# Performance work log

Measured on AMD Instinct MI355X. Metric: run time of the kernel, lower is better.

## Reference

```python
import jax, jax.numpy as jnp
import numpy as np

ESP = 1e-10  # matches SRKNN.ESP
K = 16       # top-k neighbors


def _logmap(x):
    # sign-preserving log map (repo helper not shown; eps matches SRKNN.ESP)
    return jnp.sign(x) * jnp.log(jnp.abs(x) + ESP)


def setup_inputs() -> dict:
    key = jax.random.key(0)
    k1, k2, k3, k4 = jax.random.split(key, 4)
    B, C, H, W = 2, 128, 32, 32
    C2 = C // 2
    X = jax.random.normal(k1, (B, C, H, W), jnp.float32)
    # nn.Linear(C, C//2, bias=False) weights, torch layout [out, in]
    W_min = jax.random.normal(k2, (C2, C), jnp.float32) * 0.08
    W_sub = jax.random.normal(k3, (C2, C), jnp.float32) * 0.08
    M = jax.random.normal(k4, (C2, C2), jnp.float32)
    return {"X": X, "W_min": W_min, "W_sub": W_sub, "M": M}


def reference(X, W_min, W_sub, M):
    B, C, H, W = X.shape
    XV = jnp.transpose(X, (0, 2, 3, 1)).reshape(B, -1, C)  # [B, N, C]
    N = XV.shape[1]
    # project then log-map; pairwise (i=minuend, j=subtrahend) without repeat
    pm = _logmap(XV @ W_min.T)  # [B, N, C2]
    ps = _logmap(XV @ W_sub.T)  # [B, N, C2]
    subR = jax.nn.sigmoid(pm[:, :, None, :] - ps[:, None, :, :])  # [B, N, N, C2]
    A = M.T @ M  # [C2, C2] learned Mahalanobis metric
    dis = jnp.sqrt(jnp.sum(jnp.einsum('bijc,cd->bijd', subR, A) * subR, axis=-1))  # [B,N,N]
    diff = jax.nn.sigmoid(-dis)
    value, index = jax.lax.top_k(diff, K)  # [B, N, K]
    value = -value.reshape(B, -1, 1)       # [B, N*K, 1]
    index = index.reshape(B, -1)           # [B, N*K]
    return index, value
```

## Files before the change

kernel.cpp:

```cpp
#include <hip/hip_runtime.h>
#include <hip/hip_bf16.h>
#include <hip/hip_fp16.h>
#include <math.h>

#define NN 1024
#define CC 128
#define C2 64
#define KK 16
#define NCAND 24

#if __has_builtin(__builtin_amdgcn_exp2f)
#define EXP2F(x) __builtin_amdgcn_exp2f(x)
#else
#define EXP2F(x) exp2f(x)
#endif
#define LOG2E 1.4426950408889634f

typedef __fp16  hf2   __attribute__((ext_vector_type(2)));
typedef _Float16 half8 __attribute__((ext_vector_type(8)));
typedef float f32x4    __attribute__((ext_vector_type(4)));
typedef int   int4v    __attribute__((ext_vector_type(4)));
typedef unsigned int uint;

__device__ __forceinline__ float fast_rcp(float x) {
    return __builtin_amdgcn_rcpf(x);
}

#define LDS_FENCE() do { \
    asm volatile("s_waitcnt lgkmcnt(0)" ::: "memory"); \
    __builtin_amdgcn_sched_barrier(0); } while (0)

__global__ __launch_bounds__(128) void proj_buildA(
        const float* __restrict__ X,
        const float* __restrict__ Wm,
        const float* __restrict__ Ws,
        const float* __restrict__ M,
        float* __restrict__ pm,
        float* __restrict__ ps,
        float* __restrict__ psE,
        float* __restrict__ A) {
    if (blockIdx.x >= 2 * NN) {
        const int e = (blockIdx.x - 2 * NN) * 128 + threadIdx.x;
        const int c = e >> 6, d = e & 63;
        float acc = 0.f;
        #pragma unroll 8
        for (int r = 0; r < C2; ++r)
            acc = fmaf(M[r * C2 + c], M[r * C2 + d], acc);
        A[e] = acc;
        return;
    }

    const int bn = blockIdx.x;
    const int b  = bn >> 10;
    const int n  = bn & (NN - 1);
    const int t  = threadIdx.x;

    __shared__ float xv[CC];
    xv[t] = X[b * CC * NN + t * NN + n];
    __syncthreads();

    const int d = t & (C2 - 1);
    const float* wr = ((t < C2) ? Wm : Ws) + d * CC;
    float acc = 0.f;
    #pragma unroll
    for (int c = 0; c < CC; ++c)
        acc = fmaf(wr[c], xv[c], acc);

    float a = __fadd_rn(fabsf(acc), 1e-10f);
    float l = logf(a);
    float r = (acc > 0.f) ? l : ((acc < 0.f) ? -l : 0.f);
    if (t < C2) {
        pm[bn * C2 + d] = r;
    } else {
        ps[bn * C2 + d] = r;
        psE[bn * C2 + d] = EXP2F(r * LOG2E);
    }
}

#define SIGF16(PMEF, Y0, Y1, BF) do {                                         \
    float s0 = PMEF[0] * fast_rcp(PMEF[0] + (Y0).x);                          \
    float s1 = PMEF[1] * fast_rcp(PMEF[1] + (Y0).y);                          \
    float s2 = PMEF[2] * fast_rcp(PMEF[2] + (Y0).z);                          \
    float s3 = PMEF[3] * fast_rcp(PMEF[3] + (Y0).w);                          \
    float s4 = PMEF[4] * fast_rcp(PMEF[4] + (Y1).x);                          \
    float s5 = PMEF[5] * fast_rcp(PMEF[5] + (Y1).y);                          \
    float s6 = PMEF[6] * fast_rcp(PMEF[6] + (Y1).z);                          \
    float s7 = PMEF[7] * fast_rcp(PMEF[7] + (Y1).w);                          \
    hf2 p0 = __builtin_amdgcn_cvt_pkrtz(s0, s1);                              \
    hf2 p1 = __builtin_amdgcn_cvt_pkrtz(s2, s3);                              \
    hf2 p2 = __builtin_amdgcn_cvt_pkrtz(s4, s5);                              \
    hf2 p3 = __builtin_amdgcn_cvt_pkrtz(s6, s7);                              \
    int4v iv = { __builtin_bit_cast(int, p0), __builtin_bit_cast(int, p1),    \
                 __builtin_bit_cast(int, p2), __builtin_bit_cast(int, p3) };  \
    BF = __builtin_bit_cast(half8, iv);                                       \
} while (0)

#define MFMA4(AC, KT, B)                                                              \
    AC[0] = __builtin_amdgcn_mfma_f32_16x16x32_f16(af[0][KT], B, AC[0], 0, 0, 0);     \
    AC[1] = __builtin_amdgcn_mfma_f32_16x16x32_f16(af[1][KT], B, AC[1], 0, 0, 0);     \
    AC[2] = __builtin_amdgcn_mfma_f32_16x16x32_f16(af[2][KT], B, AC[2], 0, 0, 0);     \
    AC[3] = __builtin_amdgcn_mfma_f32_16x16x32_f16(af[3][KT], B, AC[3], 0, 0, 0);

#define STREAM(PMEF, T0, T1, T2, T3, AC) do {                                 \
    half8 b0, b1;                                                             \
    SIGF16(PMEF[0], T0, T1, b0);                                              \
    SIGF16(PMEF[1], T2, T3, b1);                                              \
    MFMA4(AC, 0, b0)                                                          \
    MFMA4(AC, 1, b1)                                                          \
} while (0)

#define SQUARE16(AC, S) do {                                                  \
    _Pragma("unroll")                                                         \
    for (int e = 0; e < 4; ++e) {                                             \
        S = fmaf(AC[0][e], AC[0][e], S);                                      \
        S = fmaf(AC[1][e], AC[1][e], S);                                      \
        S = fmaf(AC[2][e], AC[2][e], S);                                      \
        S = fmaf(AC[3][e], AC[3][e], S);                                      \
    }                                                                         \
} while (0)

__global__ __launch_bounds__(256, 2) void pair_topk(
        const float* __restrict__ pm,
        const float* __restrict__ ps,
        const float* __restrict__ psE,
        const float* __restrict__ Mf,
        const float* __restrict__ A,
        float* __restrict__ out) {
    const int tid  = threadIdx.x;
    const int wv   = tid >> 6;
    const int lane = tid & 63;
    const int g    = lane >> 4;
    const int lj   = lane & 15;

    const int rbase = blockIdx.x * 4;
    const int b     = rbase >> 10;

    __shared__ uint  d2u[4][NN];
    __shared__ float sC[4][2][C2];
    __shared__ float cdiffL[4][NCAND];

    const float* psb  = ps  + b * NN * C2;
    const float* psEb = psE + b * NN * C2;

    {
        float pmEf[4][2][8];
        #pragma unroll
        for (int r = 0; r < 4; ++r) {
            #pragma unroll
            for (int kt = 0; kt < 2; ++kt) {
                const float4 a0 = *(const float4*)(pm + (rbase + r) * C2 + kt * 32 + g * 8);
                const float4 a1 = *(const float4*)(pm + (rbase + r) * C2 + kt * 32 + g * 8 + 4);
                pmEf[r][kt][0] = EXP2F(a0.x * LOG2E); pmEf[r][kt][1] = EXP2F(a0.y * LOG2E);
                pmEf[r][kt][2] = EXP2F(a0.z * LOG2E); pmEf[r][kt][3] = EXP2F(a0.w * LOG2E);
                pmEf[r][kt][4] = EXP2F(a1.x * LOG2E); pmEf[r][kt][5] = EXP2F(a1.y * LOG2E);
                pmEf[r][kt][6] = EXP2F(a1.z * LOG2E); pmEf[r][kt][7] = EXP2F(a1.w * LOG2E);
            }
        }

        half8 af[4][2];
        #pragma unroll
        for (int rt = 0; rt < 4; ++rt) {
            #pragma unroll
            for (int kt = 0; kt < 2; ++kt) {
                const float* mrow = Mf + (rt * 16 + lj) * C2 + kt * 32 + g * 8;
                const float4 m0 = *(const float4*)mrow;
                const float4 m1 = *(const float4*)(mrow + 4);
                float mv[8] = {m0.x, m0.y, m0.z, m0.w, m1.x, m1.y, m1.z, m1.w};
                #pragma unroll
                for (int e = 0; e < 8; ++e)
                    af[rt][kt][e] = (_Float16)mv[e];
            }
        }

        const int tbase = wv * 16;
        const float* p0 = psEb + (long)((tbase + 0) * 16 + lj) * C2 + g * 8;
        float4 c0 = *(const float4*)(p0);      float4 c1 = *(const float4*)(p0 + 4);
        float4 c2 = *(const float4*)(p0 + 32); float4 c3 = *(const float4*)(p0 + 36);

        #pragma unroll 1
        for (int it = 0; it < 16; ++it) {
            float4 n0, n1, n2, n3;
            if (it < 15) {
                const float* q0 = psEb + (long)((tbase + it + 1) * 16 + lj) * C2 + g * 8;
                n0 = *(const float4*)(q0);      n1 = *(const float4*)(q0 + 4);
                n2 = *(const float4*)(q0 + 32); n3 = *(const float4*)(q0 + 36);
            }

            f32x4 ac0[4] = {{0,0,0,0},{0,0,0,0},{0,0,0,0},{0,0,0,0}};
            f32x4 ac1[4] = {{0,0,0,0},{0,0,0,0},{0,0,0,0},{0,0,0,0}};
            f32x4 ac2[4] = {{0,0,0,0},{0,0,0,0},{0,0,0,0},{0,0,0,0}};
            f32x4 ac3[4] = {{0,0,0,0},{0,0,0,0},{0,0,0,0},{0,0,0,0}};

            __builtin_amdgcn_s_setprio(1);
            STREAM(pmEf[0], c0, c1, c2, c3, ac0);
            STREAM(pmEf[1], c0, c1, c2, c3, ac1);
            STREAM(pmEf[2], c0, c1, c2, c3, ac2);
            STREAM(pmEf[3], c0, c1, c2, c3, ac3);
            __builtin_amdgcn_s_setprio(0);

            float s0 = 0.f, s1 = 0.f, s2 = 0.f, s3 = 0.f;
            SQUARE16(ac0, s0);
            SQUARE16(ac1, s1);
            SQUARE16(ac2, s2);
            SQUARE16(ac3, s3);
            s0 += __shfl_xor(s0, 16, 64); s0 += __shfl_xor(s0, 32, 64);
            s1 += __shfl_xor(s1, 16, 64); s1 += __shfl_xor(s1, 32, 64);
            s2 += __shfl_xor(s2, 16, 64); s2 += __shfl_xor(s2, 32, 64);
            s3 += __shfl_xor(s3, 16, 64); s3 += __shfl_xor(s3, 32, 64);
            if (lane < 16) {
                const int jj = (tbase + it) * 16 + lane;
                d2u[0][jj] = (__float_as_uint(s0) & 0xFFFFFC00u) | (uint)jj;
                d2u[1][jj] = (__float_as_uint(s1) & 0xFFFFFC00u) | (uint)jj;
                d2u[2][jj] = (__float_as_uint(s2) & 0xFFFFFC00u) | (uint)jj;
                d2u[3][jj] = (__float_as_uint(s3) & 0xFFFFFC00u) | (uint)jj;
            }

            c0 = n0; c1 = n1; c2 = n2; c3 = n3;
        }
    }
    __syncthreads();

    const int bi = rbase + wv;
    const int i  = bi & (NN - 1);
    const float pm_own = pm[bi * C2 + lane];

    uint v[16];
    #pragma unroll
    for (int q = 0; q < 16; ++q) v[q] = d2u[wv][q * 64 + lane];

    int myCand = 0;
    #pragma unroll 1
    for (int k = 0; k < NCAND; ++k) {
        uint bv = v[0];
        #pragma unroll
        for (int q = 1; q < 16; ++q) bv = min(bv, v[q]);
        #pragma unroll
        for (int st = 0; st < 6; ++st)
            bv = min(bv, (uint)__shfl_xor((int)bv, 1 << st, 64));
        #pragma unroll
        for (int q = 0; q < 16; ++q)
            if (v[q] == bv) v[q] = 0xFFFFFFFFu;
        if (lane == k) myCand = (int)(bv & 0x3FFu);
    }

    float Acol[C2];
    #pragma unroll
    for (int c = 0; c < C2; ++c) Acol[c] = A[c * C2 + lane];

    int jvv[NCAND];
    #pragma unroll
    for (int t = 0; t < NCAND; ++t) jvv[t] = __shfl(myCand, t, 64);
    float pscv[NCAND];
    #pragma unroll
    for (int t = 0; t < NCAND; ++t) pscv[t] = psb[(long)jvv[t] * C2 + lane];

    #pragma unroll 1
    for (int t = 0; t < NCAND; t += 2) {
        float e0 = expf(pscv[t]     - pm_own);
        float e1 = expf(pscv[t + 1] - pm_own);
        float sA = 1.0f / __fadd_rn(1.0f, e0);
        float sB = 1.0f / __fadd_rn(1.0f, e1);
        sC[wv][0][lane] = sA;
        sC[wv][1][lane] = sB;
        LDS_FENCE();
        float wd0 = 0.f, wd1 = 0.f;
        #pragma unroll
        for (int c = 0; c < C2; ++c) {
            wd0 = fmaf(sC[wv][0][c], Acol[c], wd0);
            wd1 = fmaf(sC[wv][1][c], Acol[c], wd1);
        }
        const float t0 = __fmul_rn(wd0, sA);
        const float t1 = __fmul_rn(wd1, sB);
        float r80 = t0, r81 = t1;
        #pragma unroll
        for (int blk = 1; blk < 8; ++blk) {
            r80 = __fadd_rn(r80, __shfl(t0, (lane & 7) + 8 * blk, 64));
            r81 = __fadd_rn(r81, __shfl(t1, (lane & 7) + 8 * blk, 64));
        }
        float dis2a = __fadd_rn(
            __fadd_rn(__fadd_rn(__shfl(r80, 0, 64), __shfl(r80, 1, 64)),
                      __fadd_rn(__shfl(r80, 2, 64), __shfl(r80, 3, 64))),
            __fadd_rn(__fadd_rn(__shfl(r80, 4, 64), __shfl(r80, 5, 64)),
                      __fadd_rn(__shfl(r80, 6, 64), __shfl(r80, 7, 64))));
        float dis2b = __fadd_rn(
            __fadd_rn(__fadd_rn(__shfl(r81, 0, 64), __shfl(r81, 1, 64)),
                      __fadd_rn(__shfl(r81, 2, 64), __shfl(r81, 3, 64))),
            __fadd_rn(__fadd_rn(__shfl(r81, 4, 64), __shfl(r81, 5, 64)),
                      __fadd_rn(__shfl(r81, 6, 64), __shfl(r81, 7, 64))));
        float cda = 1.0f / __fadd_rn(1.0f, expf(sqrtf(dis2a)));
        float cdb = 1.0f / __fadd_rn(1.0f, expf(sqrtf(dis2b)));
        if (lane == 0) {
            cdiffL[wv][t]     = cda;
            cdiffL[wv][t + 1] = cdb;
        }
    }
    LDS_FENCE();

    float myd = (lane < NCAND) ? cdiffL[wv][lane] : -2.0f;
    int myj = (lane < NCAND) ? myCand : (1 << 20);

    const int obase = b * (NN * KK) + i * KK;
    const int vbase = 2 * NN * KK + obase;

    #pragma unroll 1
    for (int k = 0; k < KK; ++k) {
        float bd = myd;
        int bj = myj;
        #pragma unroll
        for (int st = 0; st < 6; ++st) {
            int msk = 1 << st;
            float od = __shfl_xor(bd, msk, 64);
            int oj = __shfl_xor(bj, msk, 64);
            bool better = (od > bd) || (od == bd && oj < bj);
            bd = better ? od : bd;
            bj = better ? oj : bj;
        }
        if (myj == bj) myd = -2.0f;
        if (lane == 0) {
            out[obase + k] = (float)bj;
            out[vbase + k] = -bd;
        }
    }
}

extern "C" void kernel_launch(void* const* d_in, const int* in_sizes, int n_in,
                              void* d_out, int out_size, void* d_ws, size_t ws_size,
                              hipStream_t stream) {
    const float* X  = (const float*)d_in[0];
    const float* Wm = (const float*)d_in[1];
    const float* Ws = (const float*)d_in[2];
    const float* M  = (const float*)d_in[3];

    float* A   = (float*)d_ws;
    float* pm  = A + C2 * C2;
    float* ps  = pm + 2 * NN * C2;
    float* psE = ps + 2 * NN * C2;
    float* out = (float*)d_out;

    hipLaunchKernelGGL(proj_buildA, dim3(2 * NN + 32), dim3(128), 0, stream,
                       X, Wm, Ws, M, pm, ps, psE, A);
    hipLaunchKernelGGL(pair_topk, dim3(512), dim3(256), 0, stream,
                       pm, ps, psE, M, A, out);
}
```

Baseline: 88.56 us.

## Split pair_topk work across eight waves per block instead of four

```diff
diff --git a/kernel.cpp b/kernel.cpp
--- a/kernel.cpp
+++ b/kernel.cpp
@@ -119,7 +119,7 @@
     }                                                                         \
 } while (0)
 
-__global__ __launch_bounds__(256, 2) void pair_topk(
+__global__ __launch_bounds__(512, 4) void pair_topk(
         const float* __restrict__ pm,
         const float* __restrict__ ps,
         const float* __restrict__ psE,
@@ -127,34 +127,41 @@
         const float* __restrict__ A,
         float* __restrict__ out) {
     const int tid  = threadIdx.x;
-    const int wv   = tid >> 6;
+    const int wv8  = tid >> 6;
     const int lane = tid & 63;
     const int g    = lane >> 4;
     const int lj   = lane & 15;
+    const int hf   = wv8 >> 2;
+    const int qt   = wv8 & 3;
 
     const int rbase = blockIdx.x * 4;
     const int b     = rbase >> 10;
 
     __shared__ uint  d2u[4][NN];
-    __shared__ float sC[4][2][C2];
+    __shared__ float sC[8][2][C2];
     __shared__ float cdiffL[4][NCAND];
 
     const float* psb  = ps  + b * NN * C2;
     const float* psEb = psE + b * NN * C2;
 
     {
-        float pmEf[4][2][8];
-        #pragma unroll
-        for (int r = 0; r < 4; ++r) {
-            #pragma unroll
-            for (int kt = 0; kt < 2; ++kt) {
-                const float4 a0 = *(const float4*)(pm + (rbase + r) * C2 + kt * 32 + g * 8);
-                const float4 a1 = *(const float4*)(pm + (rbase + r) * C2 + kt * 32 + g * 8 + 4);
-                pmEf[r][kt][0] = EXP2F(a0.x * LOG2E); pmEf[r][kt][1] = EXP2F(a0.y * LOG2E);
-                pmEf[r][kt][2] = EXP2F(a0.z * LOG2E); pmEf[r][kt][3] = EXP2F(a0.w * LOG2E);
-                pmEf[r][kt][4] = EXP2F(a1.x * LOG2E); pmEf[r][kt][5] = EXP2F(a1.y * LOG2E);
-                pmEf[r][kt][6] = EXP2F(a1.z * LOG2E); pmEf[r][kt][7] = EXP2F(a1.w * LOG2E);
-            }
+        const int r0 = rbase + hf * 2;
+
+        float pmEf0[2][8], pmEf1[2][8];
+        #pragma unroll
+        for (int kt = 0; kt < 2; ++kt) {
+            const float4 a0 = *(const float4*)(pm + r0 * C2 + kt * 32 + g * 8);
+            const float4 a1 = *(const float4*)(pm + r0 * C2 + kt * 32 + g * 8 + 4);
+            pmEf0[kt][0] = EXP2F(a0.x * LOG2E); pmEf0[kt][1] = EXP2F(a0.y * LOG2E);
+            pmEf0[kt][2] = EXP2F(a0.z * LOG2E); pmEf0[kt][3] = EXP2F(a0.w * LOG2E);
+            pmEf0[kt][4] = EXP2F(a1.x * LOG2E); pmEf0[kt][5] = EXP2F(a1.y * LOG2E);
+            pmEf0[kt][6] = EXP2F(a1.z * LOG2E); pmEf0[kt][7] = EXP2F(a1.w * LOG2E);
+            const float4 c0 = *(const float4*)(pm + (r0 + 1) * C2 + kt * 32 + g * 8);
+            const float4 c1 = *(const float4*)(pm + (r0 + 1) * C2 + kt * 32 + g * 8 + 4);
+            pmEf1[kt][0] = EXP2F(c0.x * LOG2E); pmEf1[kt][1] = EXP2F(c0.y * LOG2E);
+            pmEf1[kt][2] = EXP2F(c0.z * LOG2E); pmEf1[kt][3] = EXP2F(c0.w * LOG2E);
+            pmEf1[kt][4] = EXP2F(c1.x * LOG2E); pmEf1[kt][5] = EXP2F(c1.y * LOG2E);
+            pmEf1[kt][6] = EXP2F(c1.z * LOG2E); pmEf1[kt][7] = EXP2F(c1.w * LOG2E);
         }
 
         half8 af[4][2];
@@ -172,61 +179,45 @@
             }
         }
 
-        const int tbase = wv * 16;
-        const float* p0 = psEb + (long)((tbase + 0) * 16 + lj) * C2 + g * 8;
-        float4 c0 = *(const float4*)(p0);      float4 c1 = *(const float4*)(p0 + 4);
-        float4 c2 = *(const float4*)(p0 + 32); float4 c3 = *(const float4*)(p0 + 36);
+        const int tbase = qt * 16;
 
         #pragma unroll 1
         for (int it = 0; it < 16; ++it) {
-            float4 n0, n1, n2, n3;
-            if (it < 15) {
-                const float* q0 = psEb + (long)((tbase + it + 1) * 16 + lj) * C2 + g * 8;
-                n0 = *(const float4*)(q0);      n1 = *(const float4*)(q0 + 4);
-                n2 = *(const float4*)(q0 + 32); n3 = *(const float4*)(q0 + 36);
-            }
+            const float* pj = psEb + (long)((tbase + it) * 16 + lj) * C2 + g * 8;
+            const float4 c0 = *(const float4*)(pj);
+            const float4 c1 = *(const float4*)(pj + 4);
+            const float4 c2 = *(const float4*)(pj + 32);
+            const float4 c3 = *(const float4*)(pj + 36);
 
             f32x4 ac0[4] = {{0,0,0,0},{0,0,0,0},{0,0,0,0},{0,0,0,0}};
             f32x4 ac1[4] = {{0,0,0,0},{0,0,0,0},{0,0,0,0},{0,0,0,0}};
-            f32x4 ac2[4] = {{0,0,0,0},{0,0,0,0},{0,0,0,0},{0,0,0,0}};
-            f32x4 ac3[4] = {{0,0,0,0},{0,0,0,0},{0,0,0,0},{0,0,0,0}};
 
             __builtin_amdgcn_s_setprio(1);
-            STREAM(pmEf[0], c0, c1, c2, c3, ac0);
-            STREAM(pmEf[1], c0, c1, c2, c3, ac1);
-            STREAM(pmEf[2], c0, c1, c2, c3, ac2);
-            STREAM(pmEf[3], c0, c1, c2, c3, ac3);
+            STREAM(pmEf0, c0, c1, c2, c3, ac0);
+            STREAM(pmEf1, c0, c1, c2, c3, ac1);
             __builtin_amdgcn_s_setprio(0);
 
-            float s0 = 0.f, s1 = 0.f, s2 = 0.f, s3 = 0.f;
+            float s0 = 0.f, s1 = 0.f;
             SQUARE16(ac0, s0);
             SQUARE16(ac1, s1);
-            SQUARE16(ac2, s2);
-            SQUARE16(ac3, s3);
             s0 += __shfl_xor(s0, 16, 64); s0 += __shfl_xor(s0, 32, 64);
             s1 += __shfl_xor(s1, 16, 64); s1 += __shfl_xor(s1, 32, 64);
-            s2 += __shfl_xor(s2, 16, 64); s2 += __shfl_xor(s2, 32, 64);
-            s3 += __shfl_xor(s3, 16, 64); s3 += __shfl_xor(s3, 32, 64);
             if (lane < 16) {
                 const int jj = (tbase + it) * 16 + lane;
-                d2u[0][jj] = (__float_as_uint(s0) & 0xFFFFFC00u) | (uint)jj;
-                d2u[1][jj] = (__float_as_uint(s1) & 0xFFFFFC00u) | (uint)jj;
-                d2u[2][jj] = (__float_as_uint(s2) & 0xFFFFFC00u) | (uint)jj;
-                d2u[3][jj] = (__float_as_uint(s3) & 0xFFFFFC00u) | (uint)jj;
+                d2u[hf * 2 + 0][jj] = (__float_as_uint(s0) & 0xFFFFFC00u) | (uint)jj;
+                d2u[hf * 2 + 1][jj] = (__float_as_uint(s1) & 0xFFFFFC00u) | (uint)jj;
             }
-
-            c0 = n0; c1 = n1; c2 = n2; c3 = n3;
         }
     }
     __syncthreads();
 
-    const int bi = rbase + wv;
+    const int bi = rbase + qt;
     const int i  = bi & (NN - 1);
     const float pm_own = pm[bi * C2 + lane];
 
     uint v[16];
     #pragma unroll
-    for (int q = 0; q < 16; ++q) v[q] = d2u[wv][q * 64 + lane];
+    for (int q = 0; q < 16; ++q) v[q] = d2u[qt][q * 64 + lane];
 
     int myCand = 0;
     #pragma unroll 1
@@ -247,27 +238,28 @@
     #pragma unroll
     for (int c = 0; c < C2; ++c) Acol[c] = A[c * C2 + lane];
 
-    int jvv[NCAND];
-    #pragma unroll
-    for (int t = 0; t < NCAND; ++t) jvv[t] = __shfl(myCand, t, 64);
-    float pscv[NCAND];
-    #pragma unroll
-    for (int t = 0; t < NCAND; ++t) pscv[t] = psb[(long)jvv[t] * C2 + lane];
+    int jvv[12];
+    #pragma unroll
+    for (int t = 0; t < 12; ++t) jvv[t] = __shfl(myCand, hf * 12 + t, 64);
+    float pscv[12];
+    #pragma unroll
+    for (int t = 0; t < 12; ++t) pscv[t] = psb[(long)jvv[t] * C2 + lane];
 
     #pragma unroll 1
-    for (int t = 0; t < NCAND; t += 2) {
-        float e0 = expf(pscv[t]     - pm_own);
-        float e1 = expf(pscv[t + 1] - pm_own);
+    for (int tt = 0; tt < 12; tt += 2) {
+        const int t = hf * 12 + tt;
+        float e0 = expf(pscv[tt]     - pm_own);
+        float e1 = expf(pscv[tt + 1] - pm_own);
         float sA = 1.0f / __fadd_rn(1.0f, e0);
         float sB = 1.0f / __fadd_rn(1.0f, e1);
-        sC[wv][0][lane] = sA;
-        sC[wv][1][lane] = sB;
+        sC[wv8][0][lane] = sA;
+        sC[wv8][1][lane] = sB;
         LDS_FENCE();
         float wd0 = 0.f, wd1 = 0.f;
         #pragma unroll
         for (int c = 0; c < C2; ++c) {
-            wd0 = fmaf(sC[wv][0][c], Acol[c], wd0);
-            wd1 = fmaf(sC[wv][1][c], Acol[c], wd1);
+            wd0 = fmaf(sC[wv8][0][c], Acol[c], wd0);
+            wd1 = fmaf(sC[wv8][1][c], Acol[c], wd1);
         }
         const float t0 = __fmul_rn(wd0, sA);
         const float t1 = __fmul_rn(wd1, sB);
@@ -290,35 +282,37 @@
         float cda = 1.0f / __fadd_rn(1.0f, expf(sqrtf(dis2a)));
         float cdb = 1.0f / __fadd_rn(1.0f, expf(sqrtf(dis2b)));
         if (lane == 0) {
-            cdiffL[wv][t]     = cda;
-            cdiffL[wv][t + 1] = cdb;
-        }
-    }
-    LDS_FENCE();
-
-    float myd = (lane < NCAND) ? cdiffL[wv][lane] : -2.0f;
-    int myj = (lane < NCAND) ? myCand : (1 << 20);
-
-    const int obase = b * (NN * KK) + i * KK;
-    const int vbase = 2 * NN * KK + obase;
-
-    #pragma unroll 1
-    for (int k = 0; k < KK; ++k) {
-        float bd = myd;
-        int bj = myj;
-        #pragma unroll
-        for (int st = 0; st < 6; ++st) {
-            int msk = 1 << st;
-            float od = __shfl_xor(bd, msk, 64);
-            int oj = __shfl_xor(bj, msk, 64);
-            bool better = (od > bd) || (od == bd && oj < bj);
-            bd = better ? od : bd;
-            bj = better ? oj : bj;
-        }
-        if (myj == bj) myd = -2.0f;
-        if (lane == 0) {
-            out[obase + k] = (float)bj;
-            out[vbase + k] = -bd;
+            cdiffL[qt][t]     = cda;
+            cdiffL[qt][t + 1] = cdb;
+        }
+    }
+    __syncthreads();
+
+    if (hf == 0) {
+        float myd = (lane < NCAND) ? cdiffL[qt][lane] : -2.0f;
+        int myj = (lane < NCAND) ? myCand : (1 << 20);
+
+        const int obase = b * (NN * KK) + i * KK;
+        const int vbase = 2 * NN * KK + obase;
+
+        #pragma unroll 1
+        for (int k = 0; k < KK; ++k) {
+            float bd = myd;
+            int bj = myj;
+            #pragma unroll
+            for (int st = 0; st < 6; ++st) {
+                int msk = 1 << st;
+                float od = __shfl_xor(bd, msk, 64);
+                int oj = __shfl_xor(bj, msk, 64);
+                bool better = (od > bd) || (od == bd && oj < bj);
+                bd = better ? od : bd;
+                bj = better ? oj : bj;
+            }
+            if (myj == bj) myd = -2.0f;
+            if (lane == 0) {
+                out[obase + k] = (float)bj;
+                out[vbase + k] = -bd;
+            }
         }
     }
 }
@@ -339,6 +333,6 @@
 
     hipLaunchKernelGGL(proj_buildA, dim3(2 * NN + 32), dim3(128), 0, stream,
                        X, Wm, Ws, M, pm, ps, psE, A);
-    hipLaunchKernelGGL(pair_topk, dim3(512), dim3(256), 0, stream,
+    hipLaunchKernelGGL(pair_topk, dim3(512), dim3(512), 0, stream,
                        pm, ps, psE, M, A, out);
 }
```

Result: slower. 95.89 us (+8.3%).
